# Optimization experiments

Hardware: AMD Instinct MI355X
Metric: run time of the kernel (lower is better)

The kernel has to match this reference:

```python
import jax, jax.numpy as jnp
import numpy as np

B = 1      # layer math only broadcasts for batch_size == 1
E = 384    # encoding_len = prod(input_shape[1:])


def setup_inputs() -> dict:
    key = jax.random.key(0)
    k1, k2, k3 = jax.random.split(key, 3)
    x = jax.random.normal(k1, (B, E), dtype=jnp.float32)
    kernel = jax.random.normal(k2, (B, E, E * E), dtype=jnp.float32) * 0.02
    bias = jax.random.normal(k3, (E, E * E), dtype=jnp.float32) * 0.02
    space = jnp.zeros((B, E, E * E), dtype=jnp.float32)  # persistent state, init zeros
    return {"x": x, "kernel": kernel, "bias": bias, "space": space}


def reference(x, kernel, bias, space):
    Bv, Ev = x.shape
    I = jnp.eye(Ev, dtype=x.dtype)
    inv_sqrt2 = jnp.asarray(1.0 / np.sqrt(2.0), dtype=x.dtype)
    # kron(x_flat (1,E), I (E,E)) -> (E, E*E): kron[k, j*E+l] = x[0,j] * I[k,l]
    # batched form: [b,k,j,l] = x[b,j] * I[k,l], then flatten (j,l) -> E*E columns
    kron = jnp.einsum('bj,kl->bkjl', x, I).reshape(Bv, Ev, Ev * Ev) * inv_sqrt2
    updated_space = space + kernel * kron + bias[None, :, :]
    # einsum 'bQW,bQ->bQW': scale each row Q of the memory by the input entry
    target = updated_space * x[:, :, None]
    # softmax over axis=1 (rows E), then max over the E*E columns
    out = jnp.max(jax.nn.softmax(target, axis=1), axis=-1)
    return out.reshape(Bv, Ev)
```

## Files before the change

kernel.cpp:

```cpp
#include <hip/hip_runtime.h>
#include <hip/hip_bf16.h>
#include <math.h>


#define E   384
#define CW  (E * E)
#define CB  32
#define CBP 33
#define NWG (CW / CB)
#define TPB 512
#define WB  18
#define KB  6

__device__ __forceinline__ unsigned enc_f32(float v) {
    unsigned u = __float_as_uint(v);
    return (u & 0x80000000u) ? ~u : (u | 0x80000000u);
}
__device__ __forceinline__ float dec_f32(unsigned e) {
    unsigned u = (e & 0x80000000u) ? (e ^ 0x80000000u) : ~e;
    return __uint_as_float(u);
}

__global__ __launch_bounds__(TPB, 6) void gm_main(
    const float* __restrict__ x, const float* __restrict__ kern,
    const float* __restrict__ bias, const float* __restrict__ space,
    float* __restrict__ pw, unsigned* __restrict__ aws, int use_atomic)
{
    __shared__ float tile[E * CBP];
    __shared__ float pm[256];
    __shared__ float ps[256];
    __shared__ float Lc[CB];

    const int t  = threadIdx.x;
    const int wg = blockIdx.x;
    const int c0 = wg * CB;
    const int j  = c0 / E;
    const int ls = c0 % E;
    const float xj = x[j] * 0.70710678118654752440f;

    const int g  = t & 7;
    const int rb = t >> 3;
    #pragma unroll 3
    for (int i = 0; i < 6; ++i) {
        const int r = rb + 64 * i;
        const int base = r * CW + c0 + 4 * g;
        const float4 b4 = *(const float4*)(bias + base);
        const float4 s4 = *(const float4*)(space + base);
        float v0 = b4.x + s4.x, v1 = b4.y + s4.y;
        float v2 = b4.z + s4.z, v3 = b4.w + s4.w;
        const int cl = r - ls;
        if (cl >= 4 * g && cl < 4 * g + 4) {
            const float kd = kern[r * CW + c0 + cl] * xj;
            if      (cl == 4 * g)     v0 += kd;
            else if (cl == 4 * g + 1) v1 += kd;
            else if (cl == 4 * g + 2) v2 += kd;
            else                      v3 += kd;
        }
        const float xr = x[r];
        float* dst = tile + r * CBP + 4 * g;
        dst[0] = v0 * xr; dst[1] = v1 * xr; dst[2] = v2 * xr; dst[3] = v3 * xr;
    }
    __syncthreads();

    {
        const int col = t & 31;
        const int r0  = (t >> 5) * 24;
        float m = -INFINITY;
        for (int r = r0; r < r0 + 24; ++r)
            m = fmaxf(m, tile[r * CBP + col]);
        float s = 0.f;
        for (int r = r0; r < r0 + 24; ++r)
            s += expf(tile[r * CBP + col] - m);
        const float mo = __shfl_xor(m, 32);
        const float so = __shfl_xor(s, 32);
        const float M2 = fmaxf(m, mo);
        const float S2 = s * expf(m - M2) + so * expf(mo - M2);
        if ((t & 63) < 32) {
            pm[(t >> 6) * 32 + col] = M2;
            ps[(t >> 6) * 32 + col] = S2;
        }
    }
    __syncthreads();
    if (t < CB) {
        float M = -INFINITY;
        #pragma unroll
        for (int p = 0; p < 8; ++p) M = fmaxf(M, pm[p * 32 + t]);
        float S = 0.f;
        #pragma unroll
        for (int p = 0; p < 8; ++p) S += ps[p * 32 + t] * expf(pm[p * 32 + t] - M);
        Lc[t] = M + logf(S);
    }
    __syncthreads();

    if (t < E) {
        float mx = -INFINITY;
        #pragma unroll 8
        for (int c = 0; c < CB; ++c)
            mx = fmaxf(mx, tile[t * CBP + c] - Lc[c]);
        if (use_atomic) atomicMax(aws + t, enc_f32(mx));
        else            pw[(long)wg * E + t] = mx;
    }
}

__global__ __launch_bounds__(256) void gm_reduce1(
    const float* __restrict__ pw, float* __restrict__ pw2)
{
    __shared__ float sm[256];
    const int t  = threadIdx.x;
    const int kb = blockIdx.x % KB;
    const int wb = blockIdx.x / KB;
    const int k  = kb * 64 + (t & 63);
    const int wl = t >> 6;
    float mx = -INFINITY;
    for (int w = wb * 256 + wl; w < wb * 256 + 256; w += 4)
        mx = fmaxf(mx, pw[(long)w * E + k]);
    sm[t] = mx;
    __syncthreads();
    if (t < 64) {
        mx = fmaxf(fmaxf(sm[t], sm[t + 64]), fmaxf(sm[t + 128], sm[t + 192]));
        pw2[wb * E + kb * 64 + t] = mx;
    }
}

__global__ __launch_bounds__(384) void gm_reduce2(
    const float* __restrict__ pw2, float* __restrict__ out)
{
    const int k = threadIdx.x;
    float mx = -INFINITY;
    #pragma unroll
    for (int wb = 0; wb < WB; ++wb)
        mx = fmaxf(mx, pw2[wb * E + k]);
    out[k] = expf(mx);
}

__global__ __launch_bounds__(384) void gm_final_atomic(
    const unsigned* __restrict__ aws, float* __restrict__ out)
{
    const int k = threadIdx.x;
    out[k] = expf(dec_f32(aws[k]));
}

extern "C" void kernel_launch(void* const* d_in, const int* in_sizes, int n_in,
                              void* d_out, int out_size, void* d_ws, size_t ws_size,
                              hipStream_t stream)
{
    const float* x     = (const float*)d_in[0];
    const float* kern  = (const float*)d_in[1];
    const float* bias  = (const float*)d_in[2];
    const float* space = (const float*)d_in[3];
    float* out = (float*)d_out;

    const size_t pw_elems  = (size_t)NWG * E;
    const size_t need = (pw_elems + (size_t)WB * E) * sizeof(float);

    if (ws_size >= need) {
        float* pw  = (float*)d_ws;
        float* pw2 = pw + pw_elems;
        gm_main<<<NWG, TPB, 0, stream>>>(x, kern, bias, space, pw, nullptr, 0);
        gm_reduce1<<<KB * WB, 256, 0, stream>>>(pw, pw2);
        gm_reduce2<<<1, 384, 0, stream>>>(pw2, out);
    } else {
        unsigned* aws = (unsigned*)d_ws;
        hipMemsetAsync(aws, 0, E * sizeof(unsigned), stream);
        gm_main<<<NWG, TPB, 0, stream>>>(x, kern, bias, space, nullptr, aws, 1);
        gm_final_atomic<<<1, 384, 0, stream>>>(aws, out);
    }
}
```

Baseline: 569.6 us.

## Keep per-block column tile in registers and widen column block to 64

Each workgroup now handles 64 columns instead of 32. The 384xCB tile is held in per-thread registers (12 rows by 4 columns each) rather than in LDS. The column softmax statistics are combined with wave shuffles, and the per-row max is done with a shuffle reduction across the 16 column groups. This removes most LDS traffic and one barrier, and halves the partial-result buffer and the reduction work. The cost is higher register pressure (lower occupancy target of 4) and per-row shuffle reductions with partially idle lanes writing results.

```diff
diff --git a/kernel.cpp b/kernel.cpp
--- a/kernel.cpp
+++ b/kernel.cpp
@@ -1,15 +1,14 @@
 #include <hip/hip_runtime.h>
-#include <hip/hip_bf16.h>
 #include <math.h>
 
 
 #define E   384
 #define CW  (E * E)
-#define CB  32
-#define CBP 33
+#define CB  64
 #define NWG (CW / CB)
 #define TPB 512
-#define WB  18
+#define RPT 12
+#define WB  9
 #define KB  6
 
 __device__ __forceinline__ unsigned enc_f32(float v) {
@@ -21,14 +20,13 @@
     return __uint_as_float(u);
 }
 
-__global__ __launch_bounds__(TPB, 6) void gm_main(
+__global__ __launch_bounds__(TPB, 4) void gm_main(
     const float* __restrict__ x, const float* __restrict__ kern,
     const float* __restrict__ bias, const float* __restrict__ space,
     float* __restrict__ pw, unsigned* __restrict__ aws, int use_atomic)
 {
-    __shared__ float tile[E * CBP];
-    __shared__ float pm[256];
-    __shared__ float ps[256];
+    __shared__ float pmS[8][CB];
+    __shared__ float psS[8][CB];
     __shared__ float Lc[CB];
 
     const int t  = threadIdx.x;
@@ -38,67 +36,96 @@
     const int ls = c0 % E;
     const float xj = x[j] * 0.70710678118654752440f;
 
-    const int g  = t & 7;
-    const int rb = t >> 3;
-    #pragma unroll 3
-    for (int i = 0; i < 6; ++i) {
-        const int r = rb + 64 * i;
-        const int base = r * CW + c0 + 4 * g;
+    const int cg = t & 15;
+    const int rp = t >> 4;
+    const int r0 = rp * RPT;
+    const int w  = t >> 6;
+
+    float tv[RPT][4];
+    #pragma unroll
+    for (int i = 0; i < RPT; ++i) {
+        const int r = r0 + i;
+        const long base = (long)r * CW + c0 + 4 * cg;
         const float4 b4 = *(const float4*)(bias + base);
         const float4 s4 = *(const float4*)(space + base);
         float v0 = b4.x + s4.x, v1 = b4.y + s4.y;
         float v2 = b4.z + s4.z, v3 = b4.w + s4.w;
         const int cl = r - ls;
-        if (cl >= 4 * g && cl < 4 * g + 4) {
-            const float kd = kern[r * CW + c0 + cl] * xj;
-            if      (cl == 4 * g)     v0 += kd;
-            else if (cl == 4 * g + 1) v1 += kd;
-            else if (cl == 4 * g + 2) v2 += kd;
-            else                      v3 += kd;
+        if (cl >= 4 * cg && cl < 4 * cg + 4) {
+            const float kd = kern[(long)r * CW + c0 + cl] * xj;
+            if      (cl == 4 * cg)     v0 += kd;
+            else if (cl == 4 * cg + 1) v1 += kd;
+            else if (cl == 4 * cg + 2) v2 += kd;
+            else                       v3 += kd;
         }
         const float xr = x[r];
-        float* dst = tile + r * CBP + 4 * g;
-        dst[0] = v0 * xr; dst[1] = v1 * xr; dst[2] = v2 * xr; dst[3] = v3 * xr;
+        tv[i][0] = v0 * xr; tv[i][1] = v1 * xr;
+        tv[i][2] = v2 * xr; tv[i][3] = v3 * xr;
+    }
+
+    float m[4], s[4];
+    #pragma unroll
+    for (int e = 0; e < 4; ++e) m[e] = tv[0][e];
+    #pragma unroll
+    for (int i = 1; i < RPT; ++i) {
+        #pragma unroll
+        for (int e = 0; e < 4; ++e) m[e] = fmaxf(m[e], tv[i][e]);
+    }
+    #pragma unroll
+    for (int e = 0; e < 4; ++e) s[e] = 0.f;
+    #pragma unroll
+    for (int i = 0; i < RPT; ++i) {
+        #pragma unroll
+        for (int e = 0; e < 4; ++e) s[e] += expf(tv[i][e] - m[e]);
+    }
+
+    #pragma unroll
+    for (int d = 16; d <= 32; d <<= 1) {
+        #pragma unroll
+        for (int e = 0; e < 4; ++e) {
+            const float mo = __shfl_xor(m[e], d);
+            const float so = __shfl_xor(s[e], d);
+            const float M  = fmaxf(m[e], mo);
+            s[e] = s[e] * expf(m[e] - M) + so * expf(mo - M);
+            m[e] = M;
+        }
+    }
+    if (((t >> 4) & 3) == 0) {
+        #pragma unroll
+        for (int e = 0; e < 4; ++e) {
+            pmS[w][4 * cg + e] = m[e];
+            psS[w][4 * cg + e] = s[e];
+        }
     }
     __syncthreads();
 
-    {
-        const int col = t & 31;
-        const int r0  = (t >> 5) * 24;
-        float m = -INFINITY;
-        for (int r = r0; r < r0 + 24; ++r)
-            m = fmaxf(m, tile[r * CBP + col]);
-        float s = 0.f;
-        for (int r = r0; r < r0 + 24; ++r)
-            s += expf(tile[r * CBP + col] - m);
-        const float mo = __shfl_xor(m, 32);
-        const float so = __shfl_xor(s, 32);
-        const float M2 = fmaxf(m, mo);
-        const float S2 = s * expf(m - M2) + so * expf(mo - M2);
-        if ((t & 63) < 32) {
-            pm[(t >> 6) * 32 + col] = M2;
-            ps[(t >> 6) * 32 + col] = S2;
-        }
-    }
-    __syncthreads();
     if (t < CB) {
         float M = -INFINITY;
         #pragma unroll
-        for (int p = 0; p < 8; ++p) M = fmaxf(M, pm[p * 32 + t]);
+        for (int p = 0; p < 8; ++p) M = fmaxf(M, pmS[p][t]);
         float S = 0.f;
         #pragma unroll
-        for (int p = 0; p < 8; ++p) S += ps[p * 32 + t] * expf(pm[p * 32 + t] - M);
+        for (int p = 0; p < 8; ++p) S += psS[p][t] * expf(pmS[p][t] - M);
         Lc[t] = M + logf(S);
     }
     __syncthreads();
 
-    if (t < E) {
-        float mx = -INFINITY;
-        #pragma unroll 8
-        for (int c = 0; c < CB; ++c)
-            mx = fmaxf(mx, tile[t * CBP + c] - Lc[c]);
-        if (use_atomic) atomicMax(aws + t, enc_f32(mx));
-        else            pw[(long)wg * E + t] = mx;
+    float lc[4];
+    #pragma unroll
+    for (int e = 0; e < 4; ++e) lc[e] = Lc[4 * cg + e];
+    #pragma unroll
+    for (int i = 0; i < RPT; ++i) {
+        float v = tv[i][0] - lc[0];
+        v = fmaxf(v, tv[i][1] - lc[1]);
+        v = fmaxf(v, tv[i][2] - lc[2]);
+        v = fmaxf(v, tv[i][3] - lc[3]);
+        #pragma unroll
+        for (int d = 1; d <= 8; d <<= 1)
+            v = fmaxf(v, __shfl_xor(v, d));
+        if (cg == 0) {
+            if (use_atomic) atomicMax(aws + r0 + i, enc_f32(v));
+            else            pw[(long)wg * E + r0 + i] = v;
+        }
     }
 }
 
@@ -150,7 +177,7 @@
     const float* space = (const float*)d_in[3];
     float* out = (float*)d_out;
 
-    const size_t pw_elems  = (size_t)NWG * E;
+    const size_t pw_elems = (size_t)NWG * E;
     const size_t need = (pw_elems + (size_t)WB * E) * sizeof(float);
 
     if (ws_size >= need) {
```

Measured after the change: 578.0 us. Within noise of the previous version (+1.5%).
